# Optimization experiments

Measured on AMD Instinct MI355X. Metric: run time of the kernel, lower is better.

The kernel has to match this reference:

```python
import jax, jax.numpy as jnp
import numpy as np

N = 100000      # num nodes
E = 3200000     # num edges
F = 128         # feature dim (in == out, required by final in-place copy)
U = 1000        # num_users


def gcn_conv(x, edge_index, W, b):
    """PyG GCNConv: symmetric-normalized adjacency with self-loops.
    out = D^{-1/2} (A + I) D^{-1/2} X W + b
    """
    xw = x @ W                                   # [N, F]
    src, dst = edge_index[0], edge_index[1]
    # in-degree including the self-loop (+1)
    deg = jax.ops.segment_sum(jnp.ones((E,), x.dtype), dst, num_segments=N) + 1.0
    inv_sqrt = jax.lax.rsqrt(deg)                # [N]
    coef = inv_sqrt[src] * inv_sqrt[dst]         # [E]
    agg = jax.ops.segment_sum(xw[src] * coef[:, None], dst, num_segments=N)
    # self-loop contribution: norm_ii = inv_sqrt[i]^2
    return agg + xw * (inv_sqrt * inv_sqrt)[:, None] + b


def setup_inputs() -> dict:
    key = jax.random.key(0)
    k1, k2, k3, k4, k5, k6 = jax.random.split(key, 6)
    x = jax.random.normal(k1, (N, F), dtype=jnp.float32)
    edge_index = jax.random.randint(k2, (2, E), 0, N, dtype=jnp.int64)
    s = 1.0 / np.sqrt(F)
    W1 = jax.random.normal(k3, (F, F), dtype=jnp.float32) * s
    b1 = jnp.zeros((F,), dtype=jnp.float32)
    W2 = jax.random.normal(k4, (F, F), dtype=jnp.float32) * s
    b2 = jnp.zeros((F,), dtype=jnp.float32)
    return {"x": x, "edge_index": edge_index, "W1": W1, "b1": b1, "W2": W2, "b2": b2}


def reference(x, edge_index, W1, b1, W2, b2):
    # eval mode: dropout(p=0.5, training=False) is identity; detach is a no-op in fwd
    h = jax.nn.elu(gcn_conv(x, edge_index, W1, b1))
    h = jax.nn.elu(gcn_conv(h, edge_index, W2, b2))
    # x[num_users:] = movie_features  -> movie rows restored to original input
    return jnp.concatenate([h[:U], x[U:]], axis=0)
```

## Files before the change

kernel.cpp:

```cpp
#include <hip/hip_runtime.h>


#define F_DIM 128
#define U_USERS 1000
#define NFCAP 48000
#define NCHUNK 3
#define SBIN 40960
#define SW (SBIN / 2)
#define PSLICE 85
#define BMW 3136
#define SMEM_BYTES 32768
#define NBPS 49

using f16x8 = __attribute__((ext_vector_type(8))) _Float16;
using f16x2 = __attribute__((ext_vector_type(2))) _Float16;
using f32x4 = __attribute__((ext_vector_type(4))) float;

__global__ __launch_bounds__(256) void zero_kernel(int* __restrict__ fr,
                                                   unsigned long long* __restrict__ desc,
                                                   int n) {
    int t = blockIdx.x * 256 + threadIdx.x;
    int n4 = n >> 2;
    if (t < n4) ((int4*)fr)[t] = make_int4(0, 0, 0, 0);
    if (t < (n & 3)) fr[(n & ~3) + t] = 0;
    if (t < NBPS) desc[t] = 0ull;
}

__global__ __launch_bounds__(1024) void hist_kernel(const int* __restrict__ src,
                                                    const int* __restrict__ dst,
                                                    unsigned int* __restrict__ partial,
                                                    int* __restrict__ fr, int E, int n) {
    __shared__ unsigned int h[SW];
    int tid = threadIdx.x;
    int c = blockIdx.x % NCHUNK;
    int p = blockIdx.x / NCHUNK;
    for (int i = tid; i < SW; i += 1024) h[i] = 0u;
    __syncthreads();

    int lo = c * SBIN;
    int hi = lo + SBIN;
    int len = (E + PSLICE - 1) / PSLICE;
    int base = p * len;
    int end = min(E, base + len);
    int e = base + tid * 4;
    for (; e + 3 < end; e += 4096) {
        int4 dv = *(const int4*)(dst + e);
#pragma unroll
        for (int i = 0; i < 4; ++i) {
            int d = ((const int*)&dv)[i];
            if ((unsigned)d < (unsigned)n) {
                if (d >= lo && d < hi) {
                    int local = d - lo;
                    atomicAdd(&h[local >> 1], 1u << ((local & 1) << 4));
                }
                if (c == 0 && d < U_USERS) {
                    int s = src[e + i];
                    if ((unsigned)s < (unsigned)n) fr[s] = 1;
                }
            }
        }
    }
    for (; e < end; ++e) {
        int d = dst[e];
        if ((unsigned)d < (unsigned)n) {
            if (d >= lo && d < hi) {
                int local = d - lo;
                atomicAdd(&h[local >> 1], 1u << ((local & 1) << 4));
            }
            if (c == 0 && d < U_USERS) {
                int s = src[e];
                if ((unsigned)s < (unsigned)n) fr[s] = 1;
            }
        }
    }
    __syncthreads();
    unsigned int* outp = partial + ((size_t)(c * PSLICE + p)) * SW;
    for (int i = tid; i < SW; i += 1024) outp[i] = h[i];
}

__global__ __launch_bounds__(1024) void prep_scan_kernel(
    const unsigned int* __restrict__ partial, const int* __restrict__ fr,
    float* __restrict__ inv, int* __restrict__ rp, int* __restrict__ remap,
    int* __restrict__ flist, int* __restrict__ nf_dev,
    unsigned int* __restrict__ bitsG, unsigned long long* __restrict__ desc, int n) {
    __shared__ unsigned long long ss[1024];
    __shared__ unsigned int bmw[64];
    __shared__ unsigned long long spre;
    int b = blockIdx.x, t = threadIdx.x;
    int i0 = b * 2048 + t * 2;

    unsigned a0 = 0, a1 = 0;
    {
        int c = i0 / SBIN;
        int w = (i0 - c * SBIN) >> 1;
        const unsigned int* bp = partial + (size_t)c * PSLICE * SW + w;
#pragma unroll 5
        for (int p = 0; p < PSLICE; ++p) {
            unsigned v = bp[(size_t)p * SW];
            a0 += v & 0xFFFFu; a1 += v >> 16;
        }
    }
    bool in0 = i0 < n, in1 = i0 + 1 < n;
    int fv0 = 0, fv1 = 0;
    if (in1) { int2 f2 = *(const int2*)(fr + i0); fv0 = f2.x; fv1 = f2.y; }
    else if (in0) fv0 = fr[i0];
    int isf0 = (in0 && ((i0 < U_USERS) || fv0)) ? 1 : 0;
    int isf1 = (in1 && ((i0 + 1 < U_USERS) || fv1)) ? 1 : 0;
    unsigned d0 = isf0 ? a0 : 0u, d1 = isf1 ? a1 : 0u;

    if (in1) *(float2*)(inv + i0) = make_float2(rsqrtf((float)a0 + 1.f),
                                                rsqrtf((float)a1 + 1.f));
    else if (in0) inv[i0] = rsqrtf((float)a0 + 1.f);

    if (t < 64) bmw[t] = 0u;
    __syncthreads();
    unsigned pbits = (unsigned)isf0 | ((unsigned)isf1 << 1);
    if (pbits) atomicOr(&bmw[(t * 2) >> 5], pbits << ((t * 2) & 31));
    __syncthreads();
    if (t < 64) bitsG[b * 64 + t] = bmw[t];

    unsigned long long myv = ((unsigned long long)(d0 + d1) << 20) |
                             (unsigned)(isf0 + isf1);
    ss[t] = myv;
    __syncthreads();
    for (int ofs = 1; ofs < 1024; ofs <<= 1) {
        unsigned long long v = (t >= ofs) ? ss[t - ofs] : 0ull;
        __syncthreads(); ss[t] += v; __syncthreads();
    }
    unsigned long long total = ss[1023];

    if (t == 0) atomicExch(&desc[b], (total << 1) | 1ull);
    if (t < 64) {
        int pblk = b - 1 - t;
        unsigned long long v = 0ull;
        if (pblk >= 0) {
            unsigned long long d;
            do { d = atomicAdd(&desc[pblk], 0ull); } while (!(d & 1ull));
            v = d >> 1;
        }
#pragma unroll
        for (int o = 32; o > 0; o >>= 1) v += __shfl_down(v, o);
        if (t == 0) spre = v;
    }
    __syncthreads();

    unsigned long long ex = spre + ss[t] - myv;
    int rp0 = (int)(ex >> 20), rm0 = (int)(ex & 0xFFFFFu);
    unsigned long long ex1 = ex + ((((unsigned long long)d0) << 20) | (unsigned)isf0);
    int rp1 = (int)(ex1 >> 20), rm1 = (int)(ex1 & 0xFFFFFu);
    if (in1) {
        *(int2*)(rp + i0) = make_int2(rp0, rp1);
        *(int2*)(remap + i0) = make_int2(rm0, rm1);
    } else if (in0) { rp[i0] = rp0; remap[i0] = rm0; }
    if (isf0 && rm0 < NFCAP) flist[rm0] = i0;
    if (isf1 && rm1 < NFCAP) flist[rm1] = i0 + 1;
    if (in0 && i0 == n - 1) *nf_dev = min(rp0 * 0 + rm0 + isf0, NFCAP);
    if (in1 && i0 + 1 == n - 1) *nf_dev = min(rm1 + isf1, NFCAP);
}

__device__ __forceinline__ void fill_csr_body(const int* __restrict__ src,
                                              const int* __restrict__ dst,
                                              const unsigned int* __restrict__ bitsG,
                                              int* __restrict__ rp, int* __restrict__ col,
                                              int E, int n, int fblk,
                                              unsigned char* smem) {
    unsigned int* bm = (unsigned int*)smem;
    int tid = threadIdx.x;
    int nw = (n + 31) >> 5;
    for (int i = tid; i < nw; i += 256) bm[i] = bitsG[i];
    __syncthreads();

    int t = fblk * 256 + tid;
    int e0 = t * 4;
    if (e0 + 3 < E) {
        int4 dv = *(const int4*)(dst + e0);
        int4 sv = *(const int4*)(src + e0);
        const int* dp = (const int*)&dv;
        const int* sp = (const int*)&sv;
        bool f[4];
#pragma unroll
        for (int i = 0; i < 4; ++i) {
            int d = dp[i];
            f[i] = ((unsigned)d < (unsigned)n) && ((unsigned)sp[i] < (unsigned)n)
                   && ((bm[d >> 5] >> (d & 31)) & 1u);
        }
        int pos[4];
#pragma unroll
        for (int i = 0; i < 4; ++i) {
            pos[i] = -1;
            if (f[i]) pos[i] = atomicAdd(&rp[dp[i]], 1);
        }
#pragma unroll
        for (int i = 0; i < 4; ++i) {
            if (f[i] && (unsigned)pos[i] < (unsigned)E) col[pos[i]] = sp[i];
        }
    } else {
        for (int e = e0; e < E; ++e) {
            int d = dst[e], s = src[e];
            if ((unsigned)d < (unsigned)n && (unsigned)s < (unsigned)n &&
                ((bm[d >> 5] >> (d & 31)) & 1u)) {
                int pos = atomicAdd(&rp[d], 1);
                if ((unsigned)pos < (unsigned)E) col[pos] = s;
            }
        }
    }
}

__device__ __forceinline__ void stage_wt(const float* __restrict__ W, _Float16* Wt, int tid) {
#pragma unroll
    for (int i = 0; i < 8; ++i) {
        int j = tid + 256 * i;
        int nr = j & 127;
        int k8 = j >> 7;
        f16x8 v;
#pragma unroll
        for (int kk = 0; kk < 8; ++kk)
            v[kk] = (_Float16)W[(k8 * 8 + kk) * F_DIM + nr];
        *(f16x8*)&Wt[nr * F_DIM + ((k8 ^ (nr & 15)) * 8)] = v;
    }
}

__device__ __forceinline__ void gemm_mfma_body(const float* __restrict__ X,
                                               const float* __restrict__ W,
                                               _Float16* __restrict__ outh,
                                               float* __restrict__ pout,
                                               int nrows, int rowBase,
                                               unsigned char* smem) {
    _Float16* Wt = (_Float16*)smem;
    int tid = threadIdx.x;
    stage_wt(W, Wt, tid);
    __syncthreads();

    int w = tid >> 6;
    int lane = tid & 63;
    int m = lane & 15;
    int quad = lane >> 4;
    int row = rowBase + w * 16 + m;
    bool rv = row < nrows;

    f16x8 a0, a1, a2, a3;
    {
        const float* xr = X + (size_t)row * F_DIM;
        float* pr = (pout != nullptr && rv && row >= U_USERS)
                        ? pout + (size_t)row * F_DIM : nullptr;
#pragma unroll
        for (int kc = 0; kc < 4; ++kc) {
            float4 lo = make_float4(0.f, 0.f, 0.f, 0.f);
            float4 hi = lo;
            if (rv) {
                lo = ((const float4*)(xr + kc * 32 + quad * 8))[0];
                hi = ((const float4*)(xr + kc * 32 + quad * 8))[1];
            }
            if (pr) {
                ((float4*)(pr + kc * 32 + quad * 8))[0] = lo;
                ((float4*)(pr + kc * 32 + quad * 8))[1] = hi;
            }
            f16x8 av;
            av[0] = (_Float16)lo.x; av[1] = (_Float16)lo.y;
            av[2] = (_Float16)lo.z; av[3] = (_Float16)lo.w;
            av[4] = (_Float16)hi.x; av[5] = (_Float16)hi.y;
            av[6] = (_Float16)hi.z; av[7] = (_Float16)hi.w;
            if (kc == 0) a0 = av; else if (kc == 1) a1 = av;
            else if (kc == 2) a2 = av; else a3 = av;
        }
    }

    f32x4 acc[8];
#pragma unroll
    for (int i = 0; i < 8; ++i) acc[i] = (f32x4){0.f, 0.f, 0.f, 0.f};

#pragma unroll
    for (int kc = 0; kc < 4; ++kc) {
        f16x8 a = (kc == 0) ? a0 : (kc == 1) ? a1 : (kc == 2) ? a2 : a3;
#pragma unroll
        for (int ct = 0; ct < 8; ++ct) {
            f16x8 b = *(const f16x8*)&Wt[(ct * 16 + m) * F_DIM +
                                         (((kc * 4 + quad) ^ m) * 8)];
            acc[ct] = __builtin_amdgcn_mfma_f32_16x16x32_f16(a, b, acc[ct], 0, 0, 0);
        }
    }

#pragma unroll
    for (int ct = 0; ct < 8; ++ct) {
#pragma unroll
        for (int reg = 0; reg < 4; ++reg) {
            int r = rowBase + w * 16 + quad * 4 + reg;
            if (r < nrows)
                outh[(size_t)r * F_DIM + ct * 16 + m] = (_Float16)acc[ct][reg];
        }
    }
}

__device__ __forceinline__ void gemm_mfma_body_h(const _Float16* __restrict__ Xh,
                                                 const float* __restrict__ W,
                                                 _Float16* __restrict__ outh,
                                                 int nrows, int rowBase,
                                                 unsigned char* smem) {
    _Float16* Wt = (_Float16*)smem;
    int tid = threadIdx.x;
    stage_wt(W, Wt, tid);
    __syncthreads();

    int w = tid >> 6;
    int lane = tid & 63;
    int m = lane & 15;
    int quad = lane >> 4;
    int row = rowBase + w * 16 + m;
    const _Float16* xr = Xh + (size_t)row * F_DIM;

    f32x4 acc[8];
#pragma unroll
    for (int i = 0; i < 8; ++i) acc[i] = (f32x4){0.f, 0.f, 0.f, 0.f};

#pragma unroll
    for (int kc = 0; kc < 4; ++kc) {
        f16x8 a = *(const f16x8*)(xr + kc * 32 + quad * 8);
#pragma unroll
        for (int ct = 0; ct < 8; ++ct) {
            f16x8 b = *(const f16x8*)&Wt[(ct * 16 + m) * F_DIM +
                                         (((kc * 4 + quad) ^ m) * 8)];
            acc[ct] = __builtin_amdgcn_mfma_f32_16x16x32_f16(a, b, acc[ct], 0, 0, 0);
        }
    }

#pragma unroll
    for (int ct = 0; ct < 8; ++ct) {
#pragma unroll
        for (int reg = 0; reg < 4; ++reg) {
            int r = rowBase + w * 16 + quad * 4 + reg;
            if (r < nrows)
                outh[(size_t)r * F_DIM + ct * 16 + m] = (_Float16)acc[ct][reg];
        }
    }
}

__global__ __launch_bounds__(256) void gemm_fill_kernel(const float* __restrict__ X,
                                                        const float* __restrict__ W,
                                                        _Float16* __restrict__ outh,
                                                        float* __restrict__ pout, int nrows,
                                                        int gemmBlocks, int totalBlocks,
                                                        const int* __restrict__ src,
                                                        const int* __restrict__ dst,
                                                        const unsigned int* __restrict__ bitsG,
                                                        int* __restrict__ rp,
                                                        int* __restrict__ col, int E, int n) {
    __shared__ __align__(16) unsigned char smem[SMEM_BYTES];
    int b = blockIdx.x;
    long long g = gemmBlocks, T = totalBlocks;
    int before = (int)((long long)b * g / T);
    int after  = (int)(((long long)b + 1) * g / T);
    if (after > before) {
        gemm_mfma_body(X, W, outh, pout, nrows, before * 64, smem);
    } else {
        fill_csr_body(src, dst, bitsG, rp, col, E, n, b - before, smem);
    }
}

__global__ __launch_bounds__(256) void gemm_f16_dyn_kernel(const _Float16* __restrict__ Xh,
                                                           const float* __restrict__ W,
                                                           _Float16* __restrict__ outh,
                                                           const int* __restrict__ nrows_p) {
    __shared__ __align__(16) unsigned char smem[SMEM_BYTES];
    int nrows = *nrows_p;
    int rowBase = blockIdx.x * 64;
    if (rowBase >= nrows) return;
    gemm_mfma_body_h(Xh, W, outh, nrows, rowBase, smem);
}

__global__ __launch_bounds__(256) void gather_l1_kernel(const _Float16* __restrict__ xwh,
                                                        const float* __restrict__ inv,
                                                        const int* __restrict__ rp,
                                                        const int* __restrict__ col,
                                                        const int* __restrict__ flist,
                                                        const int* __restrict__ nf_p,
                                                        const float* __restrict__ b,
                                                        _Float16* __restrict__ h1c) {
    int ci = blockIdx.x * 4 + (threadIdx.x >> 6);
    if (ci >= *nf_p) return;
    int lane = threadIdx.x & 63;
    int node = flist[ci];
    int start = (node == 0) ? 0 : rp[node - 1];
    int end = rp[node];

    float accx = 0.f, accy = 0.f;
    for (int base = start; base < end; base += 64) {
        int j = base + lane;
        int s_l = 0; float c_l = 0.f;
        if (j < end) { s_l = col[j]; c_l = inv[s_l]; }
        int cnt = min(64, end - base);
        int i = 0;
        for (; i + 8 <= cnt; i += 8) {
            int ss[8]; float ff[8]; f16x2 vv[8];
#pragma unroll
            for (int u = 0; u < 8; ++u) { ss[u] = __shfl(s_l, i + u); ff[u] = __shfl(c_l, i + u); }
#pragma unroll
            for (int u = 0; u < 8; ++u) vv[u] = ((const f16x2*)(xwh + (size_t)ss[u] * F_DIM))[lane];
#pragma unroll
            for (int u = 0; u < 8; ++u) { accx += (float)vv[u][0] * ff[u]; accy += (float)vv[u][1] * ff[u]; }
        }
        for (; i + 4 <= cnt; i += 4) {
            int ss[4]; float ff[4]; f16x2 vv[4];
#pragma unroll
            for (int u = 0; u < 4; ++u) { ss[u] = __shfl(s_l, i + u); ff[u] = __shfl(c_l, i + u); }
#pragma unroll
            for (int u = 0; u < 4; ++u) vv[u] = ((const f16x2*)(xwh + (size_t)ss[u] * F_DIM))[lane];
#pragma unroll
            for (int u = 0; u < 4; ++u) { accx += (float)vv[u][0] * ff[u]; accy += (float)vv[u][1] * ff[u]; }
        }
        for (; i < cnt; ++i) {
            int s0 = __shfl(s_l, i); float f0 = __shfl(c_l, i);
            f16x2 v0 = ((const f16x2*)(xwh + (size_t)s0 * F_DIM))[lane];
            accx += (float)v0[0] * f0;
            accy += (float)v0[1] * f0;
        }
    }

    float ivd = inv[node];
    f16x2 self = ((const f16x2*)(xwh + (size_t)node * F_DIM))[lane];
    float vx = accx * ivd + (float)self[0] * ivd * ivd + b[lane * 2];
    float vy = accy * ivd + (float)self[1] * ivd * ivd + b[lane * 2 + 1];
    vx = vx > 0.f ? vx : expf(vx) - 1.f;
    vy = vy > 0.f ? vy : expf(vy) - 1.f;
    f16x2 o; o[0] = (_Float16)vx; o[1] = (_Float16)vy;
    ((f16x2*)(h1c + (size_t)ci * F_DIM))[lane] = o;
}

__global__ __launch_bounds__(256) void gather_l2_kernel(const _Float16* __restrict__ xwc,
                                                        const float* __restrict__ inv,
                                                        const int* __restrict__ rp,
                                                        const int* __restrict__ col,
                                                        const int* __restrict__ remap,
                                                        const float* __restrict__ b,
                                                        float* __restrict__ out) {
    int node = blockIdx.x * 4 + (threadIdx.x >> 6);
    if (node >= U_USERS) return;
    int lane = threadIdx.x & 63;
    int start = (node == 0) ? 0 : rp[node - 1];
    int end = rp[node];

    float accx = 0.f, accy = 0.f;
    for (int base = start; base < end; base += 64) {
        int j = base + lane;
        int r_l = 0; float c_l = 0.f;
        if (j < end) { int s = col[j]; c_l = inv[s]; r_l = remap[s]; }
        int cnt = min(64, end - base);
        int i = 0;
        for (; i + 8 <= cnt; i += 8) {
            int rr[8]; float ff[8]; f16x2 vv[8];
#pragma unroll
            for (int u = 0; u < 8; ++u) { rr[u] = __shfl(r_l, i + u); ff[u] = __shfl(c_l, i + u); }
#pragma unroll
            for (int u = 0; u < 8; ++u) vv[u] = ((const f16x2*)(xwc + (size_t)rr[u] * F_DIM))[lane];
#pragma unroll
            for (int u = 0; u < 8; ++u) { accx += (float)vv[u][0] * ff[u]; accy += (float)vv[u][1] * ff[u]; }
        }
        for (; i + 4 <= cnt; i += 4) {
            int rr[4]; float ff[4]; f16x2 vv[4];
#pragma unroll
            for (int u = 0; u < 4; ++u) { rr[u] = __shfl(r_l, i + u); ff[u] = __shfl(c_l, i + u); }
#pragma unroll
            for (int u = 0; u < 4; ++u) vv[u] = ((const f16x2*)(xwc + (size_t)rr[u] * F_DIM))[lane];
#pragma unroll
            for (int u = 0; u < 4; ++u) { accx += (float)vv[u][0] * ff[u]; accy += (float)vv[u][1] * ff[u]; }
        }
        for (; i < cnt; ++i) {
            int r0 = __shfl(r_l, i); float f0 = __shfl(c_l, i);
            f16x2 v0 = ((const f16x2*)(xwc + (size_t)r0 * F_DIM))[lane];
            accx += (float)v0[0] * f0;
            accy += (float)v0[1] * f0;
        }
    }

    float ivd = inv[node];
    f16x2 self = ((const f16x2*)(xwc + (size_t)node * F_DIM))[lane];
    float vx = accx * ivd + (float)self[0] * ivd * ivd + b[lane * 2];
    float vy = accy * ivd + (float)self[1] * ivd * ivd + b[lane * 2 + 1];
    vx = vx > 0.f ? vx : expf(vx) - 1.f;
    vy = vy > 0.f ? vy : expf(vy) - 1.f;
    ((float2*)(out + (size_t)node * F_DIM))[lane] = make_float2(vx, vy);
}

extern "C" void kernel_launch(void* const* d_in, const int* in_sizes, int n_in,
                              void* d_out, int out_size, void* d_ws, size_t ws_size,
                              hipStream_t stream) {
    const float* x  = (const float*)d_in[0];
    const int*   ei = (const int*)d_in[1];
    const float* W1 = (const float*)d_in[2];
    const float* b1 = (const float*)d_in[3];
    const float* W2 = (const float*)d_in[4];
    const float* b2 = (const float*)d_in[5];
    float* out = (float*)d_out;

    int n = in_sizes[0] / F_DIM;
    int E = in_sizes[1] / 2;
    const int* srcI = ei;
    const int* dstI = ei + E;

    _Float16* xwh = (_Float16*)d_ws;
    _Float16* h1c = xwh + (size_t)n * F_DIM;
    float* inv   = (float*)(h1c + (size_t)NFCAP * F_DIM);
    int* fr      = (int*)(inv + n);
    int* remap   = fr + n;
    int* rp      = remap + n;
    int* flist   = rp + n;
    int* nf_dev  = flist + NFCAP;
    int* col     = nf_dev + 16;
    unsigned int* partialH = (unsigned int*)(col + E);
    unsigned int* bitsG = partialH + (size_t)NCHUNK * PSLICE * SW;
    unsigned long long* desc = (unsigned long long*)(bitsG + BMW);

    zero_kernel<<<(n / 4 + 255) / 256, 256, 0, stream>>>(fr, desc, n);

    hist_kernel<<<NCHUNK * PSLICE, 1024, 0, stream>>>(srcI, dstI, partialH, fr, E, n);

    prep_scan_kernel<<<NBPS, 1024, 0, stream>>>(partialH, fr, inv, rp, remap,
                                                flist, nf_dev, bitsG, desc, n);

    int fillBlocks = (E / 4 + 255) / 256;
    int gemmBlocks = (n + 63) / 64;
    gemm_fill_kernel<<<fillBlocks + gemmBlocks, 256, 0, stream>>>(
        x, W1, xwh, out, n, gemmBlocks, fillBlocks + gemmBlocks,
        srcI, dstI, bitsG, rp, col, E, n);

    gather_l1_kernel<<<(NFCAP + 3) / 4, 256, 0, stream>>>(xwh, inv, rp, col, flist, nf_dev, b1, h1c);

    gemm_f16_dyn_kernel<<<(NFCAP + 63) / 64, 256, 0, stream>>>(h1c, W2, xwh, nf_dev);
    gather_l2_kernel<<<(U_USERS + 3) / 4, 256, 0, stream>>>(xwh, inv, rp, col, remap, b2, out);
}
```

Baseline: 268.9 us.

## Pre-scale GEMM outputs by inverse sqrt degree and pack histogram into 8-bit bins

The source-side normalization inv_sqrt[src] is folded into the GEMM epilogue, so each row of XW is stored pre-scaled. The gathers then only sum neighbour rows and apply the destination scale once, which drops the per-edge inv lookups and multiplies. The degree histogram now packs four 8-bit counters per word, so all destinations fit in one shared-memory array per block. That removes the three-chunk split and cuts the hist launch from 255 to 128 blocks. The risk is that an 8-bit counter overflows if one destination gets more than 255 edges within a slice. Slices now hold about 25k edges, against the 16-bit lanes used before.

```diff
diff --git a/kernel.cpp b/kernel.cpp
--- a/kernel.cpp
+++ b/kernel.cpp
@@ -4,10 +4,8 @@
 #define F_DIM 128
 #define U_USERS 1000
 #define NFCAP 48000
-#define NCHUNK 3
-#define SBIN 40960
-#define SW (SBIN / 2)
-#define PSLICE 85
+#define HW 25008
+#define PSLICE 128
 #define BMW 3136
 #define SMEM_BYTES 32768
 #define NBPS 49
@@ -30,15 +28,12 @@
                                                     const int* __restrict__ dst,
                                                     unsigned int* __restrict__ partial,
                                                     int* __restrict__ fr, int E, int n) {
-    __shared__ unsigned int h[SW];
+    __shared__ unsigned int h[HW];
     int tid = threadIdx.x;
-    int c = blockIdx.x % NCHUNK;
-    int p = blockIdx.x / NCHUNK;
-    for (int i = tid; i < SW; i += 1024) h[i] = 0u;
-    __syncthreads();
-
-    int lo = c * SBIN;
-    int hi = lo + SBIN;
+    int p = blockIdx.x;
+    for (int i = tid; i < HW; i += 1024) h[i] = 0u;
+    __syncthreads();
+
     int len = (E + PSLICE - 1) / PSLICE;
     int base = p * len;
     int end = min(E, base + len);
@@ -49,12 +44,9 @@
         for (int i = 0; i < 4; ++i) {
             int d = ((const int*)&dv)[i];
             if ((unsigned)d < (unsigned)n) {
-                if (d >= lo && d < hi) {
-                    int local = d - lo;
-                    atomicAdd(&h[local >> 1], 1u << ((local & 1) << 4));
-                }
-                if (c == 0 && d < U_USERS) {
-                    int s = src[e + i];
+                atomicAdd(&h[d >> 2], 1u << ((d & 3) << 3));
+                if (d < U_USERS) {
+                    int s = dst == src ? 0 : src[e + i];
                     if ((unsigned)s < (unsigned)n) fr[s] = 1;
                 }
             }
@@ -63,44 +55,42 @@
     for (; e < end; ++e) {
         int d = dst[e];
         if ((unsigned)d < (unsigned)n) {
-            if (d >= lo && d < hi) {
-                int local = d - lo;
-                atomicAdd(&h[local >> 1], 1u << ((local & 1) << 4));
-            }
-            if (c == 0 && d < U_USERS) {
+            atomicAdd(&h[d >> 2], 1u << ((d & 3) << 3));
+            if (d < U_USERS) {
                 int s = src[e];
                 if ((unsigned)s < (unsigned)n) fr[s] = 1;
             }
         }
     }
     __syncthreads();
-    unsigned int* outp = partial + ((size_t)(c * PSLICE + p)) * SW;
-    for (int i = tid; i < SW; i += 1024) outp[i] = h[i];
+    unsigned int* outp = partial + (size_t)p * HW;
+    for (int i = tid; i < HW; i += 1024) outp[i] = h[i];
 }
 
 __global__ __launch_bounds__(1024) void prep_scan_kernel(
     const unsigned int* __restrict__ partial, const int* __restrict__ fr,
     float* __restrict__ inv, int* __restrict__ rp, int* __restrict__ remap,
-    int* __restrict__ flist, int* __restrict__ nf_dev,
+    int* __restrict__ flist, float* __restrict__ invc, int* __restrict__ nf_dev,
     unsigned int* __restrict__ bitsG, unsigned long long* __restrict__ desc, int n) {
     __shared__ unsigned long long ss[1024];
     __shared__ unsigned int bmw[64];
     __shared__ unsigned long long spre;
     int b = blockIdx.x, t = threadIdx.x;
     int i0 = b * 2048 + t * 2;
+    bool in0 = i0 < n, in1 = i0 + 1 < n;
 
     unsigned a0 = 0, a1 = 0;
-    {
-        int c = i0 / SBIN;
-        int w = (i0 - c * SBIN) >> 1;
-        const unsigned int* bp = partial + (size_t)c * PSLICE * SW + w;
-#pragma unroll 5
+    if (in0) {
+        int w = i0 >> 2;
+        int sh = (i0 & 2) * 8;
+        const unsigned int* bp = partial + w;
+#pragma unroll 8
         for (int p = 0; p < PSLICE; ++p) {
-            unsigned v = bp[(size_t)p * SW];
-            a0 += v & 0xFFFFu; a1 += v >> 16;
-        }
-    }
-    bool in0 = i0 < n, in1 = i0 + 1 < n;
+            unsigned v = bp[(size_t)p * HW];
+            a0 += (v >> sh) & 0xFFu;
+            a1 += (v >> (sh + 8)) & 0xFFu;
+        }
+    }
     int fv0 = 0, fv1 = 0;
     if (in1) { int2 f2 = *(const int2*)(fr + i0); fv0 = f2.x; fv1 = f2.y; }
     else if (in0) fv0 = fr[i0];
@@ -108,9 +98,10 @@
     int isf1 = (in1 && ((i0 + 1 < U_USERS) || fv1)) ? 1 : 0;
     unsigned d0 = isf0 ? a0 : 0u, d1 = isf1 ? a1 : 0u;
 
-    if (in1) *(float2*)(inv + i0) = make_float2(rsqrtf((float)a0 + 1.f),
-                                                rsqrtf((float)a1 + 1.f));
-    else if (in0) inv[i0] = rsqrtf((float)a0 + 1.f);
+    float r0v = rsqrtf((float)a0 + 1.f);
+    float r1v = rsqrtf((float)a1 + 1.f);
+    if (in1) *(float2*)(inv + i0) = make_float2(r0v, r1v);
+    else if (in0) inv[i0] = r0v;
 
     if (t < 64) bmw[t] = 0u;
     __syncthreads();
@@ -152,9 +143,9 @@
         *(int2*)(rp + i0) = make_int2(rp0, rp1);
         *(int2*)(remap + i0) = make_int2(rm0, rm1);
     } else if (in0) { rp[i0] = rp0; remap[i0] = rm0; }
-    if (isf0 && rm0 < NFCAP) flist[rm0] = i0;
-    if (isf1 && rm1 < NFCAP) flist[rm1] = i0 + 1;
-    if (in0 && i0 == n - 1) *nf_dev = min(rp0 * 0 + rm0 + isf0, NFCAP);
+    if (isf0 && rm0 < NFCAP) { flist[rm0] = i0;     invc[rm0] = r0v; }
+    if (isf1 && rm1 < NFCAP) { flist[rm1] = i0 + 1; invc[rm1] = r1v; }
+    if (in0 && i0 == n - 1) *nf_dev = min(rm0 + isf0, NFCAP);
     if (in1 && i0 + 1 == n - 1) *nf_dev = min(rm1 + isf1, NFCAP);
 }
 
@@ -222,6 +213,7 @@
 
 __device__ __forceinline__ void gemm_mfma_body(const float* __restrict__ X,
                                                const float* __restrict__ W,
+                                               const float* __restrict__ rowscale,
                                                _Float16* __restrict__ outh,
                                                float* __restrict__ pout,
                                                int nrows, int rowBase,
@@ -280,19 +272,27 @@
         }
     }
 
+    float iv4[4];
+#pragma unroll
+    for (int reg = 0; reg < 4; ++reg) {
+        int r = rowBase + w * 16 + quad * 4 + reg;
+        iv4[reg] = (r < nrows) ? rowscale[r] : 0.f;
+    }
+
 #pragma unroll
     for (int ct = 0; ct < 8; ++ct) {
 #pragma unroll
         for (int reg = 0; reg < 4; ++reg) {
             int r = rowBase + w * 16 + quad * 4 + reg;
             if (r < nrows)
-                outh[(size_t)r * F_DIM + ct * 16 + m] = (_Float16)acc[ct][reg];
+                outh[(size_t)r * F_DIM + ct * 16 + m] = (_Float16)(acc[ct][reg] * iv4[reg]);
         }
     }
 }
 
 __device__ __forceinline__ void gemm_mfma_body_h(const _Float16* __restrict__ Xh,
                                                  const float* __restrict__ W,
+                                                 const float* __restrict__ rowscale,
                                                  _Float16* __restrict__ outh,
                                                  int nrows, int rowBase,
                                                  unsigned char* smem) {
@@ -323,19 +323,27 @@
         }
     }
 
+    float iv4[4];
+#pragma unroll
+    for (int reg = 0; reg < 4; ++reg) {
+        int r = rowBase + w * 16 + quad * 4 + reg;
+        iv4[reg] = (r < nrows) ? rowscale[r] : 0.f;
+    }
+
 #pragma unroll
     for (int ct = 0; ct < 8; ++ct) {
 #pragma unroll
         for (int reg = 0; reg < 4; ++reg) {
             int r = rowBase + w * 16 + quad * 4 + reg;
             if (r < nrows)
-                outh[(size_t)r * F_DIM + ct * 16 + m] = (_Float16)acc[ct][reg];
+                outh[(size_t)r * F_DIM + ct * 16 + m] = (_Float16)(acc[ct][reg] * iv4[reg]);
         }
     }
 }
 
 __global__ __launch_bounds__(256) void gemm_fill_kernel(const float* __restrict__ X,
                                                         const float* __restrict__ W,
+                                                        const float* __restrict__ inv,
                                                         _Float16* __restrict__ outh,
                                                         float* __restrict__ pout, int nrows,
                                                         int gemmBlocks, int totalBlocks,
@@ -350,7 +358,7 @@
     int before = (int)((long long)b * g / T);
     int after  = (int)(((long long)b + 1) * g / T);
     if (after > before) {
-        gemm_mfma_body(X, W, outh, pout, nrows, before * 64, smem);
+        gemm_mfma_body(X, W, inv, outh, pout, nrows, before * 64, smem);
     } else {
         fill_csr_body(src, dst, bitsG, rp, col, E, n, b - before, smem);
     }
@@ -358,13 +366,14 @@
 
 __global__ __launch_bounds__(256) void gemm_f16_dyn_kernel(const _Float16* __restrict__ Xh,
                                                            const float* __restrict__ W,
+                                                           const float* __restrict__ invc,
                                                            _Float16* __restrict__ outh,
                                                            const int* __restrict__ nrows_p) {
     __shared__ __align__(16) unsigned char smem[SMEM_BYTES];
     int nrows = *nrows_p;
     int rowBase = blockIdx.x * 64;
     if (rowBase >= nrows) return;
-    gemm_mfma_body_h(Xh, W, outh, nrows, rowBase, smem);
+    gemm_mfma_body_h(Xh, W, invc, outh, nrows, rowBase, smem);
 }
 
 __global__ __launch_bounds__(256) void gather_l1_kernel(const _Float16* __restrict__ xwh,
@@ -385,40 +394,40 @@
     float accx = 0.f, accy = 0.f;
     for (int base = start; base < end; base += 64) {
         int j = base + lane;
-        int s_l = 0; float c_l = 0.f;
-        if (j < end) { s_l = col[j]; c_l = inv[s_l]; }
+        int s_l = 0;
+        if (j < end) s_l = col[j];
         int cnt = min(64, end - base);
         int i = 0;
         for (; i + 8 <= cnt; i += 8) {
-            int ss[8]; float ff[8]; f16x2 vv[8];
-#pragma unroll
-            for (int u = 0; u < 8; ++u) { ss[u] = __shfl(s_l, i + u); ff[u] = __shfl(c_l, i + u); }
+            int ss[8]; f16x2 vv[8];
+#pragma unroll
+            for (int u = 0; u < 8; ++u) ss[u] = __shfl(s_l, i + u);
 #pragma unroll
             for (int u = 0; u < 8; ++u) vv[u] = ((const f16x2*)(xwh + (size_t)ss[u] * F_DIM))[lane];
 #pragma unroll
-            for (int u = 0; u < 8; ++u) { accx += (float)vv[u][0] * ff[u]; accy += (float)vv[u][1] * ff[u]; }
+            for (int u = 0; u < 8; ++u) { accx += (float)vv[u][0]; accy += (float)vv[u][1]; }
         }
         for (; i + 4 <= cnt; i += 4) {
-            int ss[4]; float ff[4]; f16x2 vv[4];
-#pragma unroll
-            for (int u = 0; u < 4; ++u) { ss[u] = __shfl(s_l, i + u); ff[u] = __shfl(c_l, i + u); }
+            int ss[4]; f16x2 vv[4];
+#pragma unroll
+            for (int u = 0; u < 4; ++u) ss[u] = __shfl(s_l, i + u);
 #pragma unroll
             for (int u = 0; u < 4; ++u) vv[u] = ((const f16x2*)(xwh + (size_t)ss[u] * F_DIM))[lane];
 #pragma unroll
-            for (int u = 0; u < 4; ++u) { accx += (float)vv[u][0] * ff[u]; accy += (float)vv[u][1] * ff[u]; }
+            for (int u = 0; u < 4; ++u) { accx += (float)vv[u][0]; accy += (float)vv[u][1]; }
         }
         for (; i < cnt; ++i) {
-            int s0 = __shfl(s_l, i); float f0 = __shfl(c_l, i);
+            int s0 = __shfl(s_l, i);
             f16x2 v0 = ((const f16x2*)(xwh + (size_t)s0 * F_DIM))[lane];
-            accx += (float)v0[0] * f0;
-            accy += (float)v0[1] * f0;
+            accx += (float)v0[0];
+            accy += (float)v0[1];
         }
     }
 
     float ivd = inv[node];
     f16x2 self = ((const f16x2*)(xwh + (size_t)node * F_DIM))[lane];
-    float vx = accx * ivd + (float)self[0] * ivd * ivd + b[lane * 2];
-    float vy = accy * ivd + (float)self[1] * ivd * ivd + b[lane * 2 + 1];
+    float vx = (accx + (float)self[0]) * ivd + b[lane * 2];
+    float vy = (accy + (float)self[1]) * ivd + b[lane * 2 + 1];
     vx = vx > 0.f ? vx : expf(vx) - 1.f;
     vy = vy > 0.f ? vy : expf(vy) - 1.f;
     f16x2 o; o[0] = (_Float16)vx; o[1] = (_Float16)vy;
@@ -441,40 +450,40 @@
     float accx = 0.f, accy = 0.f;
     for (int base = start; base < end; base += 64) {
         int j = base + lane;
-        int r_l = 0; float c_l = 0.f;
-        if (j < end) { int s = col[j]; c_l = inv[s]; r_l = remap[s]; }
+        int r_l = 0;
+        if (j < end) r_l = remap[col[j]];
         int cnt = min(64, end - base);
         int i = 0;
         for (; i + 8 <= cnt; i += 8) {
-            int rr[8]; float ff[8]; f16x2 vv[8];
-#pragma unroll
-            for (int u = 0; u < 8; ++u) { rr[u] = __shfl(r_l, i + u); ff[u] = __shfl(c_l, i + u); }
+            int rr[8]; f16x2 vv[8];
+#pragma unroll
+            for (int u = 0; u < 8; ++u) rr[u] = __shfl(r_l, i + u);
 #pragma unroll
             for (int u = 0; u < 8; ++u) vv[u] = ((const f16x2*)(xwc + (size_t)rr[u] * F_DIM))[lane];
 #pragma unroll
-            for (int u = 0; u < 8; ++u) { accx += (float)vv[u][0] * ff[u]; accy += (float)vv[u][1] * ff[u]; }
+            for (int u = 0; u < 8; ++u) { accx += (float)vv[u][0]; accy += (float)vv[u][1]; }
         }
         for (; i + 4 <= cnt; i += 4) {
-            int rr[4]; float ff[4]; f16x2 vv[4];
-#pragma unroll
-            for (int u = 0; u < 4; ++u) { rr[u] = __shfl(r_l, i + u); ff[u] = __shfl(c_l, i + u); }
+            int rr[4]; f16x2 vv[4];
+#pragma unroll
+            for (int u = 0; u < 4; ++u) rr[u] = __shfl(r_l, i + u);
 #pragma unroll
             for (int u = 0; u < 4; ++u) vv[u] = ((const f16x2*)(xwc + (size_t)rr[u] * F_DIM))[lane];
 #pragma unroll
-            for (int u = 0; u < 4; ++u) { accx += (float)vv[u][0] * ff[u]; accy += (float)vv[u][1] * ff[u]; }
+            for (int u = 0; u < 4; ++u) { accx += (float)vv[u][0]; accy += (float)vv[u][1]; }
         }
         for (; i < cnt; ++i) {
-            int r0 = __shfl(r_l, i); float f0 = __shfl(c_l, i);
+            int r0 = __shfl(r_l, i);
             f16x2 v0 = ((const f16x2*)(xwc + (size_t)r0 * F_DIM))[lane];
-            accx += (float)v0[0] * f0;
-            accy += (float)v0[1] * f0;
+            accx += (float)v0[0];
+            accy += (float)v0[1];
         }
     }
 
     float ivd = inv[node];
     f16x2 self = ((const f16x2*)(xwc + (size_t)node * F_DIM))[lane];
-    float vx = accx * ivd + (float)self[0] * ivd * ivd + b[lane * 2];
-    float vy = accy * ivd + (float)self[1] * ivd * ivd + b[lane * 2 + 1];
+    float vx = (accx + (float)self[0]) * ivd + b[lane * 2];
+    float vy = (accy + (float)self[1]) * ivd + b[lane * 2 + 1];
     vx = vx > 0.f ? vx : expf(vx) - 1.f;
     vy = vy > 0.f ? vy : expf(vy) - 1.f;
     ((float2*)(out + (size_t)node * F_DIM))[lane] = make_float2(vx, vy);
@@ -503,27 +512,28 @@
     int* remap   = fr + n;
     int* rp      = remap + n;
     int* flist   = rp + n;
-    int* nf_dev  = flist + NFCAP;
+    float* invc  = (float*)(flist + NFCAP);
+    int* nf_dev  = (int*)(invc + NFCAP);
     int* col     = nf_dev + 16;
     unsigned int* partialH = (unsigned int*)(col + E);
-    unsigned int* bitsG = partialH + (size_t)NCHUNK * PSLICE * SW;
+    unsigned int* bitsG = partialH + (size_t)PSLICE * HW;
     unsigned long long* desc = (unsigned long long*)(bitsG + BMW);
 
     zero_kernel<<<(n / 4 + 255) / 256, 256, 0, stream>>>(fr, desc, n);
 
-    hist_kernel<<<NCHUNK * PSLICE, 1024, 0, stream>>>(srcI, dstI, partialH, fr, E, n);
+    hist_kernel<<<PSLICE, 1024, 0, stream>>>(srcI, dstI, partialH, fr, E, n);
 
     prep_scan_kernel<<<NBPS, 1024, 0, stream>>>(partialH, fr, inv, rp, remap,
-                                                flist, nf_dev, bitsG, desc, n);
+                                                flist, invc, nf_dev, bitsG, desc, n);
 
     int fillBlocks = (E / 4 + 255) / 256;
     int gemmBlocks = (n + 63) / 64;
     gemm_fill_kernel<<<fillBlocks + gemmBlocks, 256, 0, stream>>>(
-        x, W1, xwh, out, n, gemmBlocks, fillBlocks + gemmBlocks,
+        x, W1, inv, xwh, out, n, gemmBlocks, fillBlocks + gemmBlocks,
         srcI, dstI, bitsG, rp, col, E, n);
 
     gather_l1_kernel<<<(NFCAP + 3) / 4, 256, 0, stream>>>(xwh, inv, rp, col, flist, nf_dev, b1, h1c);
 
-    gemm_f16_dyn_kernel<<<(NFCAP + 63) / 64, 256, 0, stream>>>(h1c, W2, xwh, nf_dev);
+    gemm_f16_dyn_kernel<<<(NFCAP + 63) / 64, 256, 0, stream>>>(h1c, W2, invc, xwh, nf_dev);
     gather_l2_kernel<<<(U_USERS + 3) / 4, 256, 0, stream>>>(xwh, inv, rp, col, remap, b2, out);
 }
```

Measured after the change: 270.2 us. No clear change (+0.5%).

## Pack degree histogram into 8-bit bins so one block covers all nodes

Applied to the files above, without the earlier changes.

The degree histogram now packs four 8-bit counters per shared-memory word, so a single block's LDS histogram spans all nodes. This removes the three destination-range chunks, and each edge slice is read once instead of three times. The grid becomes 128 slices instead of 3x85 blocks, and the prep kernel sums 128 partials per node with byte extraction. The risk is overflow of an 8-bit counter if a node receives more than 255 edges within one slice, which holds for uniform random inputs but not in general.

```diff
diff --git a/kernel.cpp b/kernel.cpp
--- a/kernel.cpp
+++ b/kernel.cpp
@@ -4,10 +4,8 @@
 #define F_DIM 128
 #define U_USERS 1000
 #define NFCAP 48000
-#define NCHUNK 3
-#define SBIN 40960
-#define SW (SBIN / 2)
-#define PSLICE 85
+#define HW 25008
+#define PSLICE 128
 #define BMW 3136
 #define SMEM_BYTES 32768
 #define NBPS 49
@@ -30,15 +28,12 @@
                                                     const int* __restrict__ dst,
                                                     unsigned int* __restrict__ partial,
                                                     int* __restrict__ fr, int E, int n) {
-    __shared__ unsigned int h[SW];
+    __shared__ unsigned int h[HW];
     int tid = threadIdx.x;
-    int c = blockIdx.x % NCHUNK;
-    int p = blockIdx.x / NCHUNK;
-    for (int i = tid; i < SW; i += 1024) h[i] = 0u;
-    __syncthreads();
-
-    int lo = c * SBIN;
-    int hi = lo + SBIN;
+    int p = blockIdx.x;
+    for (int i = tid; i < HW; i += 1024) h[i] = 0u;
+    __syncthreads();
+
     int len = (E + PSLICE - 1) / PSLICE;
     int base = p * len;
     int end = min(E, base + len);
@@ -49,11 +44,8 @@
         for (int i = 0; i < 4; ++i) {
             int d = ((const int*)&dv)[i];
             if ((unsigned)d < (unsigned)n) {
-                if (d >= lo && d < hi) {
-                    int local = d - lo;
-                    atomicAdd(&h[local >> 1], 1u << ((local & 1) << 4));
-                }
-                if (c == 0 && d < U_USERS) {
+                atomicAdd(&h[d >> 2], 1u << ((d & 3) << 3));
+                if (d < U_USERS) {
                     int s = src[e + i];
                     if ((unsigned)s < (unsigned)n) fr[s] = 1;
                 }
@@ -63,19 +55,16 @@
     for (; e < end; ++e) {
         int d = dst[e];
         if ((unsigned)d < (unsigned)n) {
-            if (d >= lo && d < hi) {
-                int local = d - lo;
-                atomicAdd(&h[local >> 1], 1u << ((local & 1) << 4));
-            }
-            if (c == 0 && d < U_USERS) {
+            atomicAdd(&h[d >> 2], 1u << ((d & 3) << 3));
+            if (d < U_USERS) {
                 int s = src[e];
                 if ((unsigned)s < (unsigned)n) fr[s] = 1;
             }
         }
     }
     __syncthreads();
-    unsigned int* outp = partial + ((size_t)(c * PSLICE + p)) * SW;
-    for (int i = tid; i < SW; i += 1024) outp[i] = h[i];
+    unsigned int* outp = partial + (size_t)p * HW;
+    for (int i = tid; i < HW; i += 1024) outp[i] = h[i];
 }
 
 __global__ __launch_bounds__(1024) void prep_scan_kernel(
@@ -88,19 +77,20 @@
     __shared__ unsigned long long spre;
     int b = blockIdx.x, t = threadIdx.x;
     int i0 = b * 2048 + t * 2;
+    bool in0 = i0 < n, in1 = i0 + 1 < n;
 
     unsigned a0 = 0, a1 = 0;
-    {
-        int c = i0 / SBIN;
-        int w = (i0 - c * SBIN) >> 1;
-        const unsigned int* bp = partial + (size_t)c * PSLICE * SW + w;
-#pragma unroll 5
+    if (in0) {
+        int w = i0 >> 2;
+        int sh = (i0 & 2) * 8;
+        const unsigned int* bp = partial + w;
+#pragma unroll 8
         for (int p = 0; p < PSLICE; ++p) {
-            unsigned v = bp[(size_t)p * SW];
-            a0 += v & 0xFFFFu; a1 += v >> 16;
-        }
-    }
-    bool in0 = i0 < n, in1 = i0 + 1 < n;
+            unsigned v = bp[(size_t)p * HW];
+            a0 += (v >> sh) & 0xFFu;
+            a1 += (v >> (sh + 8)) & 0xFFu;
+        }
+    }
     int fv0 = 0, fv1 = 0;
     if (in1) { int2 f2 = *(const int2*)(fr + i0); fv0 = f2.x; fv1 = f2.y; }
     else if (in0) fv0 = fr[i0];
@@ -108,9 +98,10 @@
     int isf1 = (in1 && ((i0 + 1 < U_USERS) || fv1)) ? 1 : 0;
     unsigned d0 = isf0 ? a0 : 0u, d1 = isf1 ? a1 : 0u;
 
-    if (in1) *(float2*)(inv + i0) = make_float2(rsqrtf((float)a0 + 1.f),
-                                                rsqrtf((float)a1 + 1.f));
-    else if (in0) inv[i0] = rsqrtf((float)a0 + 1.f);
+    float r0v = rsqrtf((float)a0 + 1.f);
+    float r1v = rsqrtf((float)a1 + 1.f);
+    if (in1) *(float2*)(inv + i0) = make_float2(r0v, r1v);
+    else if (in0) inv[i0] = r0v;
 
     if (t < 64) bmw[t] = 0u;
     __syncthreads();
@@ -154,7 +145,7 @@
     } else if (in0) { rp[i0] = rp0; remap[i0] = rm0; }
     if (isf0 && rm0 < NFCAP) flist[rm0] = i0;
     if (isf1 && rm1 < NFCAP) flist[rm1] = i0 + 1;
-    if (in0 && i0 == n - 1) *nf_dev = min(rp0 * 0 + rm0 + isf0, NFCAP);
+    if (in0 && i0 == n - 1) *nf_dev = min(rm0 + isf0, NFCAP);
     if (in1 && i0 + 1 == n - 1) *nf_dev = min(rm1 + isf1, NFCAP);
 }
 
@@ -506,12 +497,12 @@
     int* nf_dev  = flist + NFCAP;
     int* col     = nf_dev + 16;
     unsigned int* partialH = (unsigned int*)(col + E);
-    unsigned int* bitsG = partialH + (size_t)NCHUNK * PSLICE * SW;
+    unsigned int* bitsG = partialH + (size_t)PSLICE * HW;
     unsigned long long* desc = (unsigned long long*)(bitsG + BMW);
 
     zero_kernel<<<(n / 4 + 255) / 256, 256, 0, stream>>>(fr, desc, n);
 
-    hist_kernel<<<NCHUNK * PSLICE, 1024, 0, stream>>>(srcI, dstI, partialH, fr, E, n);
+    hist_kernel<<<PSLICE, 1024, 0, stream>>>(srcI, dstI, partialH, fr, E, n);
 
     prep_scan_kernel<<<NBPS, 1024, 0, stream>>>(partialH, fr, inv, rp, remap,
                                                 flist, nf_dev, bitsG, desc, n);
```

Measured after the change: 261.6 us. -2.7%, faster.
